# Optimization experiments

Measured on AMD Instinct MI355X. Metric: run time of the kernel, lower is better.

Reference implementation:

```python
import jax, jax.numpy as jnp
import numpy as np

DIM = 1024
HEADS = 16
HEAD_DIM = DIM // HEADS
B, S = 4, 2048


def setup_inputs() -> dict:
    key = jax.random.key(0)
    ks = jax.random.split(key, 12)
    scale = 1.0 / np.sqrt(DIM)
    inp = {
        "q": jax.random.normal(ks[0], (B, S, DIM), jnp.float32),
        "k": jax.random.normal(ks[1], (B, S, DIM), jnp.float32),
        "v": jax.random.normal(ks[2], (B, S, DIM), jnp.float32),
        "Wq": jax.random.normal(ks[3], (DIM, DIM), jnp.float32) * scale,
        "bq": jax.random.normal(ks[4], (DIM,), jnp.float32) * 0.01,
        "Wk": jax.random.normal(ks[5], (DIM, DIM), jnp.float32) * scale,
        "bk": jax.random.normal(ks[6], (DIM,), jnp.float32) * 0.01,
        "Wv": jax.random.normal(ks[7], (DIM, DIM), jnp.float32) * scale,
        "bv": jax.random.normal(ks[8], (DIM,), jnp.float32) * 0.01,
        "Wo": jax.random.normal(ks[9], (DIM, DIM), jnp.float32) * scale,
        "bo": jax.random.normal(ks[10], (DIM,), jnp.float32) * 0.01,
        "mask": jax.random.randint(ks[11], (B, S, S), 0, 2, jnp.int32),
    }
    return inp


def reference(q, k, v, Wq, bq, Wk, bk, Wv, bv, Wo, bo, mask):
    # QKV projections, split into heads: [B, H, S, Dh]
    def proj(x, W, b):
        y = x @ W + b
        return y.reshape(B, S, HEADS, HEAD_DIM).transpose(0, 2, 1, 3)

    qh, kh, vh = proj(q, Wq, bq), proj(k, Wk, bk), proj(v, Wv, bv)

    # scaled dot-product attention with additive mask fill (-1e9 where mask==0)
    score = jnp.einsum('bhqd,bhkd->bhqk', qh, kh) / jnp.sqrt(jnp.float32(HEAD_DIM))
    score = jnp.where(mask[:, None, :, :] == 0, jnp.float32(-1e9), score)
    attn = jax.nn.softmax(score, axis=-1)  # dropout p=0.0 -> identity

    out = jnp.einsum('bhqk,bhkd->bhqd', attn, vh)
    out = out.transpose(0, 2, 1, 3).reshape(B, S, DIM)
    return out @ Wo + bo
```

## Files before the change

kernel.cpp:

```cpp
#include <hip/hip_runtime.h>
#include <cstdint>
#include <cstddef>

#define BB 4
#define SS 2048
#define DIMM 1024
#define NH 16
#define DH 64
#define MT 8192

typedef __attribute__((ext_vector_type(8))) short bf16x8;
typedef __attribute__((ext_vector_type(4))) float f32x4;
typedef __attribute__((ext_vector_type(4))) unsigned short u16x4;
typedef __attribute__((ext_vector_type(4))) unsigned int uint32x4;

#define MFMA_BF16(a, b, c) __builtin_amdgcn_mfma_f32_16x16x32_bf16(a, b, c, 0, 0, 0)

#define QSCALE 0.1803368801111137f

__device__ __forceinline__ unsigned short f2b(float f) {
    unsigned int u = __float_as_uint(f);
    u += 0x7fffu + ((u >> 16) & 1u);
    return (unsigned short)(u >> 16);
}

__device__ __forceinline__ unsigned int cvtpk(float lo, float hi) {
    unsigned int r;
    asm("v_cvt_pk_bf16_f32 %0, %1, %2" : "=v"(r) : "v"(lo), "v"(hi));
    return r;
}

__device__ __forceinline__ float fexp2(float x) {
    float r;
    asm("v_exp_f32 %0, %1" : "=v"(r) : "v"(x));
    return r;
}

__device__ __forceinline__ void gload16(const void* g, void* l) {
    __builtin_amdgcn_global_load_lds(
        (const __attribute__((address_space(1))) unsigned int*)g,
        (__attribute__((address_space(3))) unsigned int*)l, 16, 0, 0);
}

__device__ __forceinline__ int swzb(int row, int cb) {
    return row * 128 + (((cb) ^ (row & 7)) << 4);
}

__global__ __launch_bounds__(256)
void maskpack_kernel(const int* __restrict__ m, unsigned long long* __restrict__ mp)
{
    const size_t i = (size_t)blockIdx.x * 256 + threadIdx.x;
    const unsigned long long bal = __ballot(m[i] != 0);
    if ((threadIdx.x & 63) == 0) mp[i >> 6] = bal;
}

__global__ __launch_bounds__(256)
void convert_kernel(const float* __restrict__ s0, const float* __restrict__ s1,
                    unsigned short* __restrict__ d0, unsigned short* __restrict__ d1)
{
    const float* src = blockIdx.y ? s1 : s0;
    unsigned short* dst = blockIdx.y ? d1 : d0;
    const size_t i = ((size_t)blockIdx.x * 256 + threadIdx.x) * 8;
    const float4 lo = *reinterpret_cast<const float4*>(src + i);
    const float4 hi = *reinterpret_cast<const float4*>(src + i + 4);
    uint32x4 w = {cvtpk(lo.x, lo.y), cvtpk(lo.z, lo.w),
                  cvtpk(hi.x, hi.y), cvtpk(hi.z, hi.w)};
    *reinterpret_cast<uint32x4*>(dst + i) = w;
}

__global__ __launch_bounds__(256)
void wtrans_kernel(const float* __restrict__ W, unsigned short* __restrict__ WT, float scale)
{
    __shared__ unsigned short T[64][72];
    const int tid = threadIdx.x;
    const int k0 = blockIdx.y * 64, n0 = blockIdx.x * 64;
#pragma unroll
    for (int it = 0; it < 4; ++it) {
        const int c = tid + it * 256;
        const int row = c >> 4, c4 = (c & 15) * 4;
        const float4 v = *reinterpret_cast<const float4*>(&W[(size_t)(k0 + row) * DIMM + n0 + c4]);
        T[row][c4 + 0] = f2b(v.x * scale);
        T[row][c4 + 1] = f2b(v.y * scale);
        T[row][c4 + 2] = f2b(v.z * scale);
        T[row][c4 + 3] = f2b(v.w * scale);
    }
    __syncthreads();
#pragma unroll
    for (int it = 0; it < 4; ++it) {
        const int c = tid + it * 256;
        const int n = c >> 4, k4 = (c & 15) * 4;
        u16x4 o;
        o[0] = T[k4 + 0][n];
        o[1] = T[k4 + 1][n];
        o[2] = T[k4 + 2][n];
        o[3] = T[k4 + 3][n];
        *reinterpret_cast<u16x4*>(&WT[(size_t)(n0 + n) * DIMM + k0 + k4]) = o;
    }
}

__global__ __launch_bounds__(256)
void vtrans_kernel(const unsigned short* __restrict__ Vh, unsigned short* __restrict__ VhT)
{
    __shared__ unsigned short T[64][72];
    const int tid = threadIdx.x;
    const int s0 = blockIdx.x * 64;
    const size_t base = (size_t)blockIdx.y * (size_t)(SS * DH);
#pragma unroll
    for (int it = 0; it < 2; ++it) {
        const int c = tid + it * 256;
        const int s = c >> 3, d8 = (c & 7) * 8;
        const bf16x8 v = *reinterpret_cast<const bf16x8*>(&Vh[base + (size_t)(s0 + s) * DH + d8]);
        *reinterpret_cast<bf16x8*>(&T[s][d8]) = v;
    }
    __syncthreads();
#pragma unroll
    for (int it = 0; it < 4; ++it) {
        const int c = tid + it * 256;
        const int d = c >> 4, p4 = (c & 15) * 4;
        const int cp = p4 >> 3;
        const int half = (p4 >> 2) & 1;
        const int ksrc = (cp >> 2) * 32 + (cp & 3) * 4 + half * 16;
        u16x4 o;
        o[0] = T[ksrc + 0][d];
        o[1] = T[ksrc + 1][d];
        o[2] = T[ksrc + 2][d];
        o[3] = T[ksrc + 3][d];
        *reinterpret_cast<u16x4*>(&VhT[base + (size_t)d * SS + s0 + p4]) = o;
    }
}

template<int MODE>
__global__ __launch_bounds__(256)
void gemm_kernel(const void* __restrict__ Ax, const unsigned short* __restrict__ BT,
                 const float* __restrict__ bias, void* __restrict__ Y, float bscale)
{
    __shared__ __align__(16) unsigned short As[128 * 32];
    __shared__ __align__(16) unsigned short Bs[128 * 32];
    const int tid = threadIdx.x;
    const int w = tid >> 6, l = tid & 63;
    const int g = l >> 4, li = l & 15;
    const int bid = blockIdx.x;
    const int swz = (bid & 7) * 64 + (bid >> 3);
    const int m0 = (swz >> 3) * 128, n0 = (swz & 7) * 128;
    const int wm0 = (w >> 1) * 64, wn0 = (w & 1) * 64;

    const f32x4 fzero = {0.f, 0.f, 0.f, 0.f};
    f32x4 acc[4][4];
#pragma unroll
    for (int i = 0; i < 4; ++i)
#pragma unroll
        for (int j = 0; j < 4; ++j) acc[i][j] = fzero;

    for (int k0 = 0; k0 < DIMM; k0 += 32) {
        if (MODE == 0) {
            const float* A = (const float*)Ax;
#pragma unroll
            for (int it = 0; it < 2; ++it) {
                const int c = tid + it * 256;
                const int row = c >> 2, cb = c & 3;
                const float* src = &A[(size_t)(m0 + row) * DIMM + k0 + cb * 8];
                const float4 lo = *reinterpret_cast<const float4*>(src);
                const float4 hi = *reinterpret_cast<const float4*>(src + 4);
                uint32x4 vv = {cvtpk(lo.x, lo.y), cvtpk(lo.z, lo.w),
                               cvtpk(hi.x, hi.y), cvtpk(hi.z, hi.w)};
                *reinterpret_cast<uint32x4*>(&As[c * 8]) = vv;
            }
        } else if (MODE == 3) {
            const unsigned short* A = (const unsigned short*)Ax;
#pragma unroll
            for (int it = 0; it < 2; ++it) {
                const int c = it * 256 + w * 64 + l;
                const int row = c >> 2, cb = c & 3;
                gload16(&A[(size_t)(m0 + row) * DIMM + k0 + cb * 8],
                        &As[(it * 256 + w * 64) * 8]);
            }
        } else {
            const unsigned short* A = (const unsigned short*)Ax;
            const int h = k0 >> 6;
#pragma unroll
            for (int it = 0; it < 2; ++it) {
                const int c = it * 256 + w * 64 + l;
                const int row = c >> 2, cb = c & 3;
                const int m = m0 + row;
                const int bb = m >> 11, s = m & 2047;
                const unsigned short* src =
                    &A[(((size_t)(bb * NH + h)) * SS + s) * DH + (k0 & 63) + cb * 8];
                gload16(src, &As[(it * 256 + w * 64) * 8]);
            }
        }
#pragma unroll
        for (int it = 0; it < 2; ++it) {
            const int c = it * 256 + w * 64 + l;
            const int row = c >> 2, cb = c & 3;
            const unsigned short* src = &BT[(size_t)(n0 + row) * DIMM + k0 + cb * 8];
            gload16(src, &Bs[(it * 256 + w * 64) * 8]);
        }
        __syncthreads();

        bf16x8 af[4], bf[4];
#pragma unroll
        for (int mb = 0; mb < 4; ++mb)
            af[mb] = *reinterpret_cast<const bf16x8*>(&As[(wm0 + mb * 16 + li) * 32 + g * 8]);
#pragma unroll
        for (int nb = 0; nb < 4; ++nb)
            bf[nb] = *reinterpret_cast<const bf16x8*>(&Bs[(wn0 + nb * 16 + li) * 32 + g * 8]);
#pragma unroll
        for (int mb = 0; mb < 4; ++mb)
#pragma unroll
            for (int nb = 0; nb < 4; ++nb)
                acc[mb][nb] = MFMA_BF16(af[mb], bf[nb], acc[mb][nb]);
        __syncthreads();
    }

    float bv4[4];
#pragma unroll
    for (int nb = 0; nb < 4; ++nb)
        bv4[nb] = bias[n0 + wn0 + nb * 16 + li] * bscale;

#pragma unroll
    for (int mb = 0; mb < 4; ++mb) {
#pragma unroll
        for (int r = 0; r < 4; ++r) {
            const int row_g = m0 + wm0 + mb * 16 + g * 4 + r;
#pragma unroll
            for (int nb = 0; nb < 4; ++nb) {
                const int col = n0 + wn0 + nb * 16 + li;
                const float val = acc[mb][nb][r] + bv4[nb];
                if (MODE == 1) {
                    ((float*)Y)[(size_t)row_g * DIMM + col] = val;
                } else {
                    const int bb = row_g >> 11, s = row_g & 2047;
                    const int hh = col >> 6, dd = col & 63;
                    ((unsigned short*)Y)[(((size_t)(bb * NH + hh)) * SS + s) * DH + dd] = f2b(val);
                }
            }
        }
    }
}

__global__ __launch_bounds__(256)
void flash_kernel(const unsigned short* __restrict__ Qh, const unsigned short* __restrict__ Kh,
                  const unsigned short* __restrict__ VhT, const unsigned long long* __restrict__ maskp,
                  unsigned short* __restrict__ Ctx)
{
    const int h = blockIdx.x, qt = blockIdx.y, b = blockIdx.z;
    const int tid = threadIdx.x;
    const int w = tid >> 6, l = tid & 63;
    const int g = l >> 4, li = l & 15;

    __shared__ __align__(16) unsigned short smem[4 * 64 * 64];
    __shared__ float a_arr[128], l_arr[128];

    const int q0 = qt * 128;
    const size_t hb = ((size_t)(b * NH + h)) * (size_t)(SS * DH);

    bf16x8 qf[2][2];
#pragma unroll
    for (int qc = 0; qc < 2; ++qc) {
        const unsigned short* qp = &Qh[hb + (size_t)(q0 + w * 32 + qc * 16 + li) * DH + g * 8];
        qf[qc][0] = *reinterpret_cast<const bf16x8*>(qp);
        qf[qc][1] = *reinterpret_cast<const bf16x8*>(qp + 32);
    }

    const f32x4 fzero = {0.f, 0.f, 0.f, 0.f};
    f32x4 oacc[2][4];
#pragma unroll
    for (int qc = 0; qc < 2; ++qc)
#pragma unroll
        for (int mb = 0; mb < 4; ++mb) oacc[qc][mb] = fzero;
    float mr[2] = {-3.0e38f, -3.0e38f};
    float lr[2] = {0.0f, 0.0f};

    int ks_[2], vs_[2];
#pragma unroll
    for (int it = 0; it < 2; ++it) {
        const int c = it * 256 + w * 64 + l;
        const int row = c >> 3, cb = (c & 7) ^ (row & 7);
        ks_[it] = row * DH + cb * 8;
        vs_[it] = row * SS + cb * 8;
    }
    const unsigned short* Ksrc = Kh + hb;
    const unsigned short* Vsrc = VhT + hb;
    const unsigned long long* mrow_p = maskp + ((size_t)(b * SS + q0 + w * 32 + li)) * 32;

#define STAGE(bn, tt) do {                                                      \
    gload16(Ksrc + (size_t)(tt) * 4096 + ks_[0], smem + (bn) * 4096 + w * 512); \
    gload16(Ksrc + (size_t)(tt) * 4096 + ks_[1], smem + (bn) * 4096 + 2048 + w * 512); \
    gload16(Vsrc + (size_t)(tt) * 64 + vs_[0], smem + 8192 + (bn) * 4096 + w * 512);   \
    gload16(Vsrc + (size_t)(tt) * 64 + vs_[1], smem + 8192 + (bn) * 4096 + 2048 + w * 512); \
} while (0)

    STAGE(0, 0);
    __syncthreads();

    int buf = 0;
    for (int t = 0; t < SS / 64; ++t) {
        if (t < SS / 64 - 1) STAGE(buf ^ 1, t + 1);

        const unsigned long long mw0 = mrow_p[t];
        const unsigned long long mw1 = mrow_p[512 + t];

        const char* Kc = (const char*)(smem + buf * 4096);
        bf16x8 kf[4][2];
#pragma unroll
        for (int nb = 0; nb < 4; ++nb)
#pragma unroll
            for (int hh = 0; hh < 2; ++hh)
                kf[nb][hh] = *reinterpret_cast<const bf16x8*>(
                    Kc + (nb * 16 + li) * 128 + (((hh * 4 + g) ^ (li & 7)) << 4));

        bf16x8 pf[2][2];
        bool doresc[2];
#pragma unroll
        for (int qc = 0; qc < 2; ++qc) {
            f32x4 st[4];
#pragma unroll
            for (int nb = 0; nb < 4; ++nb) st[nb] = fzero;
            __builtin_amdgcn_s_setprio(1);
#pragma unroll
            for (int nb = 0; nb < 4; ++nb)
#pragma unroll
                for (int hh = 0; hh < 2; ++hh)
                    st[nb] = MFMA_BF16(kf[nb][hh], qf[qc][hh], st[nb]);
            __builtin_amdgcn_s_setprio(0);

            const unsigned long long msh = (qc ? mw1 : mw0) >> (g * 4);
            float s[4][4];
#pragma unroll
            for (int nb = 0; nb < 4; ++nb)
#pragma unroll
                for (int r = 0; r < 4; ++r)
                    s[nb][r] = ((msh >> (nb * 16 + r)) & 1ull) ? st[nb][r] : -1.0e9f;

            float mx = s[0][0];
#pragma unroll
            for (int nb = 0; nb < 4; ++nb)
#pragma unroll
                for (int r = 0; r < 4; ++r) mx = fmaxf(mx, s[nb][r]);
            mx = fmaxf(mx, __shfl_xor(mx, 16));
            mx = fmaxf(mx, __shfl_xor(mx, 32));

            doresc[qc] = __any(mx > mr[qc] + 8.0f);
            float af = 1.0f;
            if (doresc[qc]) {
                const float mn = fmaxf(mr[qc], mx);
                af = fexp2(mr[qc] - mn);
                mr[qc] = mn;
                if (g == 0) a_arr[w * 32 + qc * 16 + li] = af;
            }

            float e[4][4];
            float ps = 0.0f;
#pragma unroll
            for (int nb = 0; nb < 4; ++nb)
#pragma unroll
                for (int r = 0; r < 4; ++r) {
                    e[nb][r] = fexp2(s[nb][r] - mr[qc]);
                    ps += e[nb][r];
                }
            ps += __shfl_xor(ps, 16);
            ps += __shfl_xor(ps, 32);
            lr[qc] = af * lr[qc] + ps;

            uint32x4 w0 = {cvtpk(e[0][0], e[0][1]), cvtpk(e[0][2], e[0][3]),
                           cvtpk(e[1][0], e[1][1]), cvtpk(e[1][2], e[1][3])};
            uint32x4 w1 = {cvtpk(e[2][0], e[2][1]), cvtpk(e[2][2], e[2][3]),
                           cvtpk(e[3][0], e[3][1]), cvtpk(e[3][2], e[3][3])};
            pf[qc][0] = __builtin_bit_cast(bf16x8, w0);
            pf[qc][1] = __builtin_bit_cast(bf16x8, w1);
        }

        const char* Vc = (const char*)(smem + 8192 + buf * 4096);
        bf16x8 vf[4][2];
#pragma unroll
        for (int mb = 0; mb < 4; ++mb)
#pragma unroll
            for (int hh = 0; hh < 2; ++hh)
                vf[mb][hh] = *reinterpret_cast<const bf16x8*>(
                    Vc + (mb * 16 + li) * 128 + (((hh * 4 + g) ^ (li & 7)) << 4));

#pragma unroll
        for (int qc = 0; qc < 2; ++qc) {
            if (doresc[qc]) {
                f32x4 av;
#pragma unroll
                for (int r = 0; r < 4; ++r) av[r] = a_arr[w * 32 + qc * 16 + g * 4 + r];
#pragma unroll
                for (int mb = 0; mb < 4; ++mb) oacc[qc][mb] = oacc[qc][mb] * av;
            }
            __builtin_amdgcn_s_setprio(1);
#pragma unroll
            for (int hh = 0; hh < 2; ++hh)
#pragma unroll
                for (int mb = 0; mb < 4; ++mb)
                    oacc[qc][mb] = MFMA_BF16(pf[qc][hh], vf[mb][hh], oacc[qc][mb]);
            __builtin_amdgcn_s_setprio(0);
        }

        __syncthreads();
        buf ^= 1;
    }
#undef STAGE

    if (g == 0) {
        l_arr[w * 32 + li] = lr[0];
        l_arr[w * 32 + 16 + li] = lr[1];
    }
    unsigned short* Ps = smem;
#pragma unroll
    for (int qc = 0; qc < 2; ++qc) {
#pragma unroll
        for (int r = 0; r < 4; ++r) {
            const int row = w * 32 + qc * 16 + g * 4 + r;
            const float linv = 1.0f / l_arr[row];
#pragma unroll
            for (int mb = 0; mb < 4; ++mb) {
                const int dd = mb * 16 + li;
                *(unsigned short*)((char*)Ps + swzb(row, dd >> 3) + (dd & 7) * 2) =
                    f2b(oacc[qc][mb][r] * linv);
            }
        }
    }
#pragma unroll
    for (int it = 0; it < 4; ++it) {
        const int c = it * 64 + l;
        const int qrow = w * 32 + (c >> 3), cb = c & 7;
        const bf16x8 ov = *reinterpret_cast<const bf16x8*>((const char*)Ps + swzb(qrow, cb));
        *reinterpret_cast<bf16x8*>(&Ctx[hb + (size_t)(q0 + qrow) * DH + cb * 8]) = ov;
    }
}

extern "C" void kernel_launch(void* const* d_in, const int* in_sizes, int n_in,
                              void* d_out, int out_size, void* d_ws, size_t ws_size,
                              hipStream_t stream)
{
    const float* q  = (const float*)d_in[0];
    const float* k  = (const float*)d_in[1];
    const float* v  = (const float*)d_in[2];
    const float* Wq = (const float*)d_in[3];
    const float* bq = (const float*)d_in[4];
    const float* Wk = (const float*)d_in[5];
    const float* bk = (const float*)d_in[6];
    const float* Wv = (const float*)d_in[7];
    const float* bv = (const float*)d_in[8];
    const float* Wo = (const float*)d_in[9];
    const float* bo = (const float*)d_in[10];
    const int* mask = (const int*)d_in[11];
    float* out = (float*)d_out;

    const size_t M1 = 1048576, M8 = (size_t)MT * DIMM;
    unsigned short* WT3 = (unsigned short*)d_ws;
    unsigned short* WTo = WT3 + 3 * M1;
    unsigned short* Qb  = WTo + M1;
    unsigned short* Kb  = Qb + M8;
    unsigned short* Qh  = Kb + M8;
    unsigned short* Kh  = Qh + M8;
    unsigned short* Vh  = Kh + M8;
    unsigned long long* maskp = (unsigned long long*)(Vh + M8);
    unsigned short* VhT = Qb;
    unsigned short* Ctx = Kb;

    dim3 blk(256);

    maskpack_kernel<<<dim3((unsigned)((size_t)BB * SS * SS / 256)), blk, 0, stream>>>(mask, maskp);

    dim3 tgrid(16, 16);
    wtrans_kernel<<<tgrid, blk, 0, stream>>>(Wq, WT3, QSCALE);
    wtrans_kernel<<<tgrid, blk, 0, stream>>>(Wk, WT3 + M1, 1.0f);
    wtrans_kernel<<<tgrid, blk, 0, stream>>>(Wv, WT3 + 2 * M1, 1.0f);
    wtrans_kernel<<<tgrid, blk, 0, stream>>>(Wo, WTo, 1.0f);

    convert_kernel<<<dim3(4096, 2), blk, 0, stream>>>(q, k, Qb, Kb);

    dim3 ggrid(512);
    gemm_kernel<3><<<ggrid, blk, 0, stream>>>(Qb, WT3, bq, Qh, QSCALE);
    gemm_kernel<3><<<ggrid, blk, 0, stream>>>(Kb, WT3 + M1, bk, Kh, 1.0f);
    gemm_kernel<0><<<ggrid, blk, 0, stream>>>(v, WT3 + 2 * M1, bv, Vh, 1.0f);

    dim3 vgrid(SS / 64, BB * NH);
    vtrans_kernel<<<vgrid, blk, 0, stream>>>(Vh, VhT);

    dim3 fgrid(NH, SS / 128, BB);
    flash_kernel<<<fgrid, blk, 0, stream>>>(Qh, Kh, VhT, maskp, Ctx);

    gemm_kernel<1><<<ggrid, blk, 0, stream>>>(Ctx, WTo, bo, out, 1.0f);
}
```

Measured before the change: 336.1 us.

## Fuse V transpose into projection epilogue and apply mask via bitwise P zeroing

```diff
diff --git a/kernel.cpp b/kernel.cpp
--- a/kernel.cpp
+++ b/kernel.cpp
@@ -56,10 +56,11 @@
 
 __global__ __launch_bounds__(256)
 void convert_kernel(const float* __restrict__ s0, const float* __restrict__ s1,
-                    unsigned short* __restrict__ d0, unsigned short* __restrict__ d1)
-{
-    const float* src = blockIdx.y ? s1 : s0;
-    unsigned short* dst = blockIdx.y ? d1 : d0;
+                    const float* __restrict__ s2, unsigned short* __restrict__ d0,
+                    unsigned short* __restrict__ d1, unsigned short* __restrict__ d2)
+{
+    const float* src = (blockIdx.y == 0) ? s0 : (blockIdx.y == 1) ? s1 : s2;
+    unsigned short* dst = (blockIdx.y == 0) ? d0 : (blockIdx.y == 1) ? d1 : d2;
     const size_t i = ((size_t)blockIdx.x * 256 + threadIdx.x) * 8;
     const float4 lo = *reinterpret_cast<const float4*>(src + i);
     const float4 hi = *reinterpret_cast<const float4*>(src + i + 4);
@@ -98,37 +99,6 @@
     }
 }
 
-__global__ __launch_bounds__(256)
-void vtrans_kernel(const unsigned short* __restrict__ Vh, unsigned short* __restrict__ VhT)
-{
-    __shared__ unsigned short T[64][72];
-    const int tid = threadIdx.x;
-    const int s0 = blockIdx.x * 64;
-    const size_t base = (size_t)blockIdx.y * (size_t)(SS * DH);
-#pragma unroll
-    for (int it = 0; it < 2; ++it) {
-        const int c = tid + it * 256;
-        const int s = c >> 3, d8 = (c & 7) * 8;
-        const bf16x8 v = *reinterpret_cast<const bf16x8*>(&Vh[base + (size_t)(s0 + s) * DH + d8]);
-        *reinterpret_cast<bf16x8*>(&T[s][d8]) = v;
-    }
-    __syncthreads();
-#pragma unroll
-    for (int it = 0; it < 4; ++it) {
-        const int c = tid + it * 256;
-        const int d = c >> 4, p4 = (c & 15) * 4;
-        const int cp = p4 >> 3;
-        const int half = (p4 >> 2) & 1;
-        const int ksrc = (cp >> 2) * 32 + (cp & 3) * 4 + half * 16;
-        u16x4 o;
-        o[0] = T[ksrc + 0][d];
-        o[1] = T[ksrc + 1][d];
-        o[2] = T[ksrc + 2][d];
-        o[3] = T[ksrc + 3][d];
-        *reinterpret_cast<u16x4*>(&VhT[base + (size_t)d * SS + s0 + p4]) = o;
-    }
-}
-
 template<int MODE>
 __global__ __launch_bounds__(256)
 void gemm_kernel(const void* __restrict__ Ax, const unsigned short* __restrict__ BT,
@@ -152,20 +122,7 @@
         for (int j = 0; j < 4; ++j) acc[i][j] = fzero;
 
     for (int k0 = 0; k0 < DIMM; k0 += 32) {
-        if (MODE == 0) {
-            const float* A = (const float*)Ax;
-#pragma unroll
-            for (int it = 0; it < 2; ++it) {
-                const int c = tid + it * 256;
-                const int row = c >> 2, cb = c & 3;
-                const float* src = &A[(size_t)(m0 + row) * DIMM + k0 + cb * 8];
-                const float4 lo = *reinterpret_cast<const float4*>(src);
-                const float4 hi = *reinterpret_cast<const float4*>(src + 4);
-                uint32x4 vv = {cvtpk(lo.x, lo.y), cvtpk(lo.z, lo.w),
-                               cvtpk(hi.x, hi.y), cvtpk(hi.z, hi.w)};
-                *reinterpret_cast<uint32x4*>(&As[c * 8]) = vv;
-            }
-        } else if (MODE == 3) {
+        if (MODE == 3 || MODE == 4) {
             const unsigned short* A = (const unsigned short*)Ax;
 #pragma unroll
             for (int it = 0; it < 2; ++it) {
@@ -228,10 +185,16 @@
                 const float val = acc[mb][nb][r] + bv4[nb];
                 if (MODE == 1) {
                     ((float*)Y)[(size_t)row_g * DIMM + col] = val;
+                } else if (MODE == 3) {
+                    const int bb = row_g >> 11, s = row_g & 2047;
+                    const int hh = col >> 6, dd = col & 63;
+                    ((unsigned short*)Y)[(((size_t)(bb * NH + hh)) * SS + s) * DH + dd] = f2b(val);
                 } else {
                     const int bb = row_g >> 11, s = row_g & 2047;
                     const int hh = col >> 6, dd = col & 63;
-                    ((unsigned short*)Y)[(((size_t)(bb * NH + hh)) * SS + s) * DH + dd] = f2b(val);
+                    const int st = s & 63;
+                    const int sp = (st & 32) + ((st >> 2) & 3) * 8 + ((st & 16) >> 2) + (st & 3);
+                    ((unsigned short*)Y)[(((size_t)(bb * NH + hh)) * DH + dd) * SS + (s & ~63) + sp] = f2b(val);
                 }
             }
         }
@@ -249,10 +212,13 @@
     const int g = l >> 4, li = l & 15;
 
     __shared__ __align__(16) unsigned short smem[4 * 64 * 64];
-    __shared__ float a_arr[128], l_arr[128];
+    __shared__ float a_arr[128];
+    __shared__ unsigned int LUT4[4];
 
     const int q0 = qt * 128;
     const size_t hb = ((size_t)(b * NH + h)) * (size_t)(SS * DH);
+
+    if (tid < 4) LUT4[tid] = ((tid & 1) ? 0xFFFFu : 0u) | ((tid & 2) ? 0xFFFF0000u : 0u);
 
     bf16x8 qf[2][2];
 #pragma unroll
@@ -262,14 +228,20 @@
         qf[qc][1] = *reinterpret_cast<const bf16x8*>(qp + 32);
     }
 
+    bf16x8 vones;
+#pragma unroll
+    for (int j = 0; j < 8; ++j) vones[j] = (short)0x3F80;
+
     const f32x4 fzero = {0.f, 0.f, 0.f, 0.f};
     f32x4 oacc[2][4];
-#pragma unroll
-    for (int qc = 0; qc < 2; ++qc)
+    f32x4 lacc[2];
+#pragma unroll
+    for (int qc = 0; qc < 2; ++qc) {
+        lacc[qc] = fzero;
 #pragma unroll
         for (int mb = 0; mb < 4; ++mb) oacc[qc][mb] = fzero;
+    }
     float mr[2] = {-3.0e38f, -3.0e38f};
-    float lr[2] = {0.0f, 0.0f};
 
     int ks_[2], vs_[2];
 #pragma unroll
@@ -324,48 +296,39 @@
                     st[nb] = MFMA_BF16(kf[nb][hh], qf[qc][hh], st[nb]);
             __builtin_amdgcn_s_setprio(0);
 
-            const unsigned long long msh = (qc ? mw1 : mw0) >> (g * 4);
-            float s[4][4];
-#pragma unroll
-            for (int nb = 0; nb < 4; ++nb)
-#pragma unroll
-                for (int r = 0; r < 4; ++r)
-                    s[nb][r] = ((msh >> (nb * 16 + r)) & 1ull) ? st[nb][r] : -1.0e9f;
-
-            float mx = s[0][0];
-#pragma unroll
-            for (int nb = 0; nb < 4; ++nb)
-#pragma unroll
-                for (int r = 0; r < 4; ++r) mx = fmaxf(mx, s[nb][r]);
+            float m0v = fmaxf(fmaxf(st[0][0], st[0][1]), fmaxf(st[0][2], st[0][3]));
+            float m1v = fmaxf(fmaxf(st[1][0], st[1][1]), fmaxf(st[1][2], st[1][3]));
+            float m2v = fmaxf(fmaxf(st[2][0], st[2][1]), fmaxf(st[2][2], st[2][3]));
+            float m3v = fmaxf(fmaxf(st[3][0], st[3][1]), fmaxf(st[3][2], st[3][3]));
+            float mx = fmaxf(fmaxf(m0v, m1v), fmaxf(m2v, m3v));
             mx = fmaxf(mx, __shfl_xor(mx, 16));
             mx = fmaxf(mx, __shfl_xor(mx, 32));
 
             doresc[qc] = __any(mx > mr[qc] + 8.0f);
-            float af = 1.0f;
             if (doresc[qc]) {
                 const float mn = fmaxf(mr[qc], mx);
-                af = fexp2(mr[qc] - mn);
+                const float af = fexp2(mr[qc] - mn);
                 mr[qc] = mn;
                 if (g == 0) a_arr[w * 32 + qc * 16 + li] = af;
             }
 
             float e[4][4];
-            float ps = 0.0f;
 #pragma unroll
             for (int nb = 0; nb < 4; ++nb)
 #pragma unroll
-                for (int r = 0; r < 4; ++r) {
-                    e[nb][r] = fexp2(s[nb][r] - mr[qc]);
-                    ps += e[nb][r];
-                }
-            ps += __shfl_xor(ps, 16);
-            ps += __shfl_xor(ps, 32);
-            lr[qc] = af * lr[qc] + ps;
-
+                for (int r = 0; r < 4; ++r)
+                    e[nb][r] = fexp2(st[nb][r] - mr[qc]);
+
+            const unsigned long long msh = (qc ? mw1 : mw0) >> (g * 4);
+            const unsigned lo = (unsigned)msh, hi = (unsigned)(msh >> 32);
             uint32x4 w0 = {cvtpk(e[0][0], e[0][1]), cvtpk(e[0][2], e[0][3]),
                            cvtpk(e[1][0], e[1][1]), cvtpk(e[1][2], e[1][3])};
             uint32x4 w1 = {cvtpk(e[2][0], e[2][1]), cvtpk(e[2][2], e[2][3]),
                            cvtpk(e[3][0], e[3][1]), cvtpk(e[3][2], e[3][3])};
+            w0[0] &= LUT4[lo & 3u];         w0[1] &= LUT4[(lo >> 2) & 3u];
+            w0[2] &= LUT4[(lo >> 16) & 3u]; w0[3] &= LUT4[(lo >> 18) & 3u];
+            w1[0] &= LUT4[hi & 3u];         w1[1] &= LUT4[(hi >> 2) & 3u];
+            w1[2] &= LUT4[(hi >> 16) & 3u]; w1[3] &= LUT4[(hi >> 18) & 3u];
             pf[qc][0] = __builtin_bit_cast(bf16x8, w0);
             pf[qc][1] = __builtin_bit_cast(bf16x8, w1);
         }
@@ -387,6 +350,7 @@
                 for (int r = 0; r < 4; ++r) av[r] = a_arr[w * 32 + qc * 16 + g * 4 + r];
 #pragma unroll
                 for (int mb = 0; mb < 4; ++mb) oacc[qc][mb] = oacc[qc][mb] * av;
+                lacc[qc] = lacc[qc] * av;
             }
             __builtin_amdgcn_s_setprio(1);
 #pragma unroll
@@ -394,6 +358,8 @@
 #pragma unroll
                 for (int mb = 0; mb < 4; ++mb)
                     oacc[qc][mb] = MFMA_BF16(pf[qc][hh], vf[mb][hh], oacc[qc][mb]);
+            lacc[qc] = MFMA_BF16(pf[qc][0], vones, lacc[qc]);
+            lacc[qc] = MFMA_BF16(pf[qc][1], vones, lacc[qc]);
             __builtin_amdgcn_s_setprio(0);
         }
 
@@ -402,17 +368,13 @@
     }
 #undef STAGE
 
-    if (g == 0) {
-        l_arr[w * 32 + li] = lr[0];
-        l_arr[w * 32 + 16 + li] = lr[1];
-    }
     unsigned short* Ps = smem;
 #pragma unroll
     for (int qc = 0; qc < 2; ++qc) {
 #pragma unroll
         for (int r = 0; r < 4; ++r) {
             const int row = w * 32 + qc * 16 + g * 4 + r;
-            const float linv = 1.0f / l_arr[row];
+            const float linv = 1.0f / lacc[qc][r];
 #pragma unroll
             for (int mb = 0; mb < 4; ++mb) {
                 const int dd = mb * 16 + li;
@@ -421,6 +383,7 @@
             }
         }
     }
+    __syncthreads();
 #pragma unroll
     for (int it = 0; it < 4; ++it) {
         const int c = it * 64 + l;
@@ -453,10 +416,10 @@
     unsigned short* WTo = WT3 + 3 * M1;
     unsigned short* Qb  = WTo + M1;
     unsigned short* Kb  = Qb + M8;
-    unsigned short* Qh  = Kb + M8;
+    unsigned short* Vb  = Kb + M8;
+    unsigned short* Qh  = Vb + M8;
     unsigned short* Kh  = Qh + M8;
-    unsigned short* Vh  = Kh + M8;
-    unsigned long long* maskp = (unsigned long long*)(Vh + M8);
+    unsigned long long* maskp = (unsigned long long*)(Kh + M8);
     unsigned short* VhT = Qb;
     unsigned short* Ctx = Kb;
 
@@ -470,15 +433,12 @@
     wtrans_kernel<<<tgrid, blk, 0, stream>>>(Wv, WT3 + 2 * M1, 1.0f);
     wtrans_kernel<<<tgrid, blk, 0, stream>>>(Wo, WTo, 1.0f);
 
-    convert_kernel<<<dim3(4096, 2), blk, 0, stream>>>(q, k, Qb, Kb);
+    convert_kernel<<<dim3(4096, 3), blk, 0, stream>>>(q, k, v, Qb, Kb, Vb);
 
     dim3 ggrid(512);
     gemm_kernel<3><<<ggrid, blk, 0, stream>>>(Qb, WT3, bq, Qh, QSCALE);
     gemm_kernel<3><<<ggrid, blk, 0, stream>>>(Kb, WT3 + M1, bk, Kh, 1.0f);
-    gemm_kernel<0><<<ggrid, blk, 0, stream>>>(v, WT3 + 2 * M1, bv, Vh, 1.0f);
-
-    dim3 vgrid(SS / 64, BB * NH);
-    vtrans_kernel<<<vgrid, blk, 0, stream>>>(Vh, VhT);
+    gemm_kernel<4><<<ggrid, blk, 0, stream>>>(Vb, WT3 + 2 * M1, bv, VhT, 1.0f);
 
     dim3 fgrid(NH, SS / 128, BB);
     flash_kernel<<<fgrid, blk, 0, stream>>>(Qh, Kh, VhT, maskp, Ctx);
```

Result: faster. 306.3 us (-8.9%).
